# Performance work log

Hardware: AMD Instinct MI355X
Metric: run time of the kernel (lower is better)

## Reference

```python
import jax, jax.numpy as jnp
import numpy as np

B, N, F, UNITS = 8, 2048, 64, 64

def setup_inputs() -> dict:
    key = jax.random.key(0)
    ks = jax.random.split(key, 7)
    inputs = jax.random.normal(ks[0], (B, N, F), dtype=jnp.float32)
    Dynamic_L = jax.random.normal(ks[1], (B, N, N), dtype=jnp.float32)
    W = jax.random.uniform(ks[2], (B, N, N, 3), dtype=jnp.float32)
    Geo = jax.random.normal(ks[3], (N, N), dtype=jnp.float32)
    KL = jax.random.normal(ks[4], (N, N), dtype=jnp.float32)
    # Dense(Units, tanh) params (glorot-ish scale)
    Wd = jax.random.normal(ks[5], (F, UNITS), dtype=jnp.float32) / np.sqrt(F)
    bd = jnp.zeros((UNITS,), dtype=jnp.float32)
    return {"inputs": inputs, "Dynamic_L": Dynamic_L, "W": W,
            "Geo": Geo, "KL": KL, "Wd": Wd, "bd": bd}

def reference(inputs, Dynamic_L, W, Geo, KL, Wd, bd):
    # Weighted fusion of three N x N matrices; Geo/KL broadcast over batch.
    Fusion = Dynamic_L * W[..., 0] + Geo[None] * W[..., 1] + KL[None] * W[..., 2]  # [B,N,N]
    Fusion = jax.nn.softmax(Fusion, axis=-1)
    G1 = jnp.einsum('bnm,bmf->bnf', Fusion, inputs)  # graph matmul [B,N,F]
    return jnp.tanh(G1 @ Wd + bd)  # Dense(Units, tanh) -> [B,N,UNITS]
```

## Files before the change

kernel.cpp:

```cpp
#include <hip/hip_runtime.h>
#include <hip/hip_fp16.h>

#define Nn 2048
#define Ff 64
#define Uu 64
#define NT 256
#define NCH 4
#define G1S 68

typedef _Float16 f16x4 __attribute__((ext_vector_type(4)));
typedef _Float16 f16x8 __attribute__((ext_vector_type(8)));
typedef float    f32x4 __attribute__((ext_vector_type(4)));

#define MFMA32(a,b,c) __builtin_amdgcn_mfma_f32_16x16x32_f16(a,b,c,0,0,0)

#define OPB   0
#define OG1A  65536
#define OG1B  69888
#define OWS   74240
#define OINV  74368
#define SMSZ  74496

__global__ __launch_bounds__(256) void transposeX(const float* __restrict__ X,
                                                  _Float16* __restrict__ Xt) {
    __shared__ _Float16 tile[64][65];
    const int b = blockIdx.x, kt = blockIdx.y;
    #pragma unroll
    for (int i = 0; i < 16; ++i) {
        int e  = i * 256 + threadIdx.x;
        int kk = e >> 6, ff = e & 63;
        tile[ff][kk] = (_Float16)X[((size_t)b * Nn + kt * 64 + kk) * Ff + ff];
    }
    __syncthreads();
    #pragma unroll
    for (int i = 0; i < 16; ++i) {
        int e  = i * 256 + threadIdx.x;
        int ff = e >> 6, kk = e & 63;
        Xt[((size_t)b * Ff + ff) * Nn + kt * 64 + kk] = tile[ff][kk];
    }
}

#define ISSUE2(d0v,d1v,gv,kv,w00,w01,w02,w10,w11,w12, C, HR) {      \
    const int _rr = (HR) >> 1;                                      \
    const size_t _o = (size_t)_rr * Nn + ((size_t)(C) << 9)         \
                    + (((HR) & 1) << 8) + (lane << 2);              \
    d0v = *(const float4*)(dR0 + _o);                               \
    d1v = *(const float4*)(dR1 + _o);                               \
    gv  = *(const float4*)(gR + _o);                                \
    kv  = *(const float4*)(kR + _o);                                \
    w00 = *(const float4*)(wR0 + 3 * _o);                           \
    w01 = *(const float4*)(wR0 + 3 * _o + 4);                       \
    w02 = *(const float4*)(wR0 + 3 * _o + 8);                       \
    w10 = *(const float4*)(wR1 + 3 * _o);                           \
    w11 = *(const float4*)(wR1 + 3 * _o + 4);                       \
    w12 = *(const float4*)(wR1 + 3 * _o + 8);                       \
}

#define CONSUME2(d0v,d1v,gv,kv,w00,w01,w02,w10,w11,w12, P0B,P1B, HR) {          \
    const int _rr = (HR) >> 1;                                                  \
    const int _tr = row0 + _rr;                                                 \
    float a0 = __expf(fminf(d0v.x*w00.x + gv.x*w00.y + kv.x*w00.z, 11.f));      \
    float a1 = __expf(fminf(d0v.y*w00.w + gv.y*w01.x + kv.y*w01.y, 11.f));      \
    float a2 = __expf(fminf(d0v.z*w01.z + gv.z*w01.w + kv.z*w02.x, 11.f));      \
    float a3 = __expf(fminf(d0v.w*w02.y + gv.w*w02.z + kv.w*w02.w, 11.f));      \
    float c0 = __expf(fminf(d1v.x*w10.x + gv.x*w10.y + kv.x*w10.z, 11.f));      \
    float c1 = __expf(fminf(d1v.y*w10.w + gv.y*w11.x + kv.y*w11.y, 11.f));      \
    float c2 = __expf(fminf(d1v.z*w11.z + gv.z*w11.w + kv.z*w12.x, 11.f));      \
    float c3 = __expf(fminf(d1v.w*w12.y + gv.w*w12.z + kv.w*w12.w, 11.f));      \
    f16x4 h0 = {(_Float16)a0, (_Float16)a1, (_Float16)a2, (_Float16)a3};        \
    f16x4 h1 = {(_Float16)c0, (_Float16)c1, (_Float16)c2, (_Float16)c3};        \
    rs0[_rr] += (float)h0[0] + (float)h0[1] + (float)h0[2] + (float)h0[3];      \
    rs1[_rr] += (float)h1[0] + (float)h1[1] + (float)h1[2] + (float)h1[3];      \
    const int _ba = (_tr * 1024 + (((HR) & 1) << 9) + (lane << 3))              \
                    ^ ((_tr & 7) << 4);                                         \
    *(f16x4*)((P0B) + _ba) = h0;                                                \
    *(f16x4*)((P1B) + _ba) = h1;                                                \
}

#define STAGE_CHUNK2(P0B, P1B, C) {                                              \
    ISSUE2(Ad0,Ad1,Agv,Akv,Aw00,Aw01,Aw02,Aw10,Aw11,Aw12, C, 0);                 \
    ISSUE2(Bd0,Bd1,Bgv,Bkv,Bw00,Bw01,Bw02,Bw10,Bw11,Bw12, C, 1);                 \
    CONSUME2(Ad0,Ad1,Agv,Akv,Aw00,Aw01,Aw02,Aw10,Aw11,Aw12, P0B,P1B, 0);         \
    ISSUE2(Ad0,Ad1,Agv,Akv,Aw00,Aw01,Aw02,Aw10,Aw11,Aw12, C, 2);                 \
    CONSUME2(Bd0,Bd1,Bgv,Bkv,Bw00,Bw01,Bw02,Bw10,Bw11,Bw12, P0B,P1B, 1);         \
    ISSUE2(Bd0,Bd1,Bgv,Bkv,Bw00,Bw01,Bw02,Bw10,Bw11,Bw12, C, 3);                 \
    CONSUME2(Ad0,Ad1,Agv,Akv,Aw00,Aw01,Aw02,Aw10,Aw11,Aw12, P0B,P1B, 2);         \
    ISSUE2(Ad0,Ad1,Agv,Akv,Aw00,Aw01,Aw02,Aw10,Aw11,Aw12, C, 4);                 \
    CONSUME2(Bd0,Bd1,Bgv,Bkv,Bw00,Bw01,Bw02,Bw10,Bw11,Bw12, P0B,P1B, 3);         \
    ISSUE2(Bd0,Bd1,Bgv,Bkv,Bw00,Bw01,Bw02,Bw10,Bw11,Bw12, C, 5);                 \
    CONSUME2(Ad0,Ad1,Agv,Akv,Aw00,Aw01,Aw02,Aw10,Aw11,Aw12, P0B,P1B, 4);         \
    ISSUE2(Ad0,Ad1,Agv,Akv,Aw00,Aw01,Aw02,Aw10,Aw11,Aw12, C, 6);                 \
    CONSUME2(Bd0,Bd1,Bgv,Bkv,Bw00,Bw01,Bw02,Bw10,Bw11,Bw12, P0B,P1B, 5);         \
    ISSUE2(Bd0,Bd1,Bgv,Bkv,Bw00,Bw01,Bw02,Bw10,Bw11,Bw12, C, 7);                 \
    CONSUME2(Ad0,Ad1,Agv,Akv,Aw00,Aw01,Aw02,Aw10,Aw11,Aw12, P0B,P1B, 6);         \
    CONSUME2(Bd0,Bd1,Bgv,Bkv,Bw00,Bw01,Bw02,Bw10,Bw11,Bw12, P0B,P1B, 7);         \
}

#define MFMA_PHASE2(PBUF, XC, ACC) {                                          \
    f16x8 p0 = *(const f16x8*)((XC));                                         \
    f16x8 p1 = *(const f16x8*)((XC) + 32);                                    \
    f16x8 p2 = *(const f16x8*)((XC) + 64);                                    \
    f16x8 p3 = *(const f16x8*)((XC) + 96);                                    \
    f16x8 p4 = *(const f16x8*)((XC) + 128);                                   \
    f16x8 p5 = *(const f16x8*)((XC) + 160);                                   \
    f16x8 p6 = *(const f16x8*)((XC) + 192);                                   \
    f16x8 p7 = *(const f16x8*)((XC) + 224);                                   \
    _Pragma("unroll")                                                         \
    for (int kk = 0; kk < 8; ++kk) {                                          \
        const int aa = r * 1024 + kk * 64 + kg * 16;                          \
        f16x8 af = *(const f16x8*)((PBUF) + (aa ^ ((r & 7) << 4)));           \
        f16x8 bv = (kk==0)?p0:(kk==1)?p1:(kk==2)?p2:(kk==3)?p3:               \
                   (kk==4)?p4:(kk==5)?p5:(kk==6)?p6:p7;                       \
        ACC = MFMA32(af, bv, ACC);                                            \
    }                                                                         \
    p0 = *(const f16x8*)((XC) + 256);                                         \
    p1 = *(const f16x8*)((XC) + 288);                                         \
    p2 = *(const f16x8*)((XC) + 320);                                         \
    p3 = *(const f16x8*)((XC) + 352);                                         \
    p4 = *(const f16x8*)((XC) + 384);                                         \
    p5 = *(const f16x8*)((XC) + 416);                                         \
    p6 = *(const f16x8*)((XC) + 448);                                         \
    p7 = *(const f16x8*)((XC) + 480);                                         \
    _Pragma("unroll")                                                         \
    for (int kk = 0; kk < 8; ++kk) {                                          \
        const int aa = r * 1024 + (kk + 8) * 64 + kg * 16;                    \
        f16x8 af = *(const f16x8*)((PBUF) + (aa ^ ((r & 7) << 4)));           \
        f16x8 bv = (kk==0)?p0:(kk==1)?p1:(kk==2)?p2:(kk==3)?p3:               \
                   (kk==4)?p4:(kk==5)?p5:(kk==6)?p6:p7;                       \
        ACC = MFMA32(af, bv, ACC);                                            \
    }                                                                         \
}

__global__ __launch_bounds__(NT, 2) void fused_gcn(
    const _Float16* __restrict__ Xt,
    const float* __restrict__ Dyn,
    const float* __restrict__ Wf,
    const float* __restrict__ Geo,
    const float* __restrict__ KLm,
    const float* __restrict__ Wd,
    const float* __restrict__ bdv,
    float* __restrict__ out)
{
    __shared__ __align__(16) char SM[SMSZ];

    const int t    = threadIdx.x;
    const int lane = t & 63;
    const int wid  = t >> 6;
    const int r    = lane & 15;
    const int kg   = lane >> 4;
    const int rg   = blockIdx.x & 127;
    const int pp   = blockIdx.x >> 7;
    const int n0   = rg << 4;
    const int b0   = pp * 2, b1 = pp * 2 + 1;
    const int row0 = wid << 2;

    const float* dR0 = Dyn + ((size_t)b0 * Nn + n0 + row0) * Nn;
    const float* dR1 = Dyn + ((size_t)b1 * Nn + n0 + row0) * Nn;
    const float* wR0 = Wf  + ((size_t)b0 * Nn + n0 + row0) * (size_t)Nn * 3;
    const float* wR1 = Wf  + ((size_t)b1 * Nn + n0 + row0) * (size_t)Nn * 3;
    const float* gR  = Geo + (size_t)(n0 + row0) * Nn;
    const float* kR  = KLm + (size_t)(n0 + row0) * Nn;
    const _Float16* xw0 = Xt + (size_t)b0 * Ff * Nn
                        + (size_t)(wid * 16 + r) * Nn + (kg << 3);
    const _Float16* xw1 = Xt + (size_t)b1 * Ff * Nn
                        + (size_t)(wid * 16 + r) * Nn + (kg << 3);

    f32x4 acc0 = {0.f,0.f,0.f,0.f}, acc1 = {0.f,0.f,0.f,0.f};
    float rs0[4] = {0.f,0.f,0.f,0.f}, rs1[4] = {0.f,0.f,0.f,0.f};
    float4 Ad0,Ad1,Agv,Akv,Aw00,Aw01,Aw02,Aw10,Aw11,Aw12;
    float4 Bd0,Bd1,Bgv,Bkv,Bw00,Bw01,Bw02,Bw10,Bw11,Bw12;

    STAGE_CHUNK2(SM + OPB, SM + OPB + 16384, 0);
    __syncthreads();

    #pragma unroll 1
    for (int c = 0; c < NCH; ++c) {
        char* bufc = SM + OPB + (c & 1) * 32768;
        MFMA_PHASE2(bufc,          xw0 + ((size_t)c << 9), acc0);
        MFMA_PHASE2(bufc + 16384,  xw1 + ((size_t)c << 9), acc1);
        if (c + 1 < NCH) {
            char* bufn = SM + OPB + ((c + 1) & 1) * 32768;
            STAGE_CHUNK2(bufn, bufn + 16384, c + 1);
        }
        __syncthreads();
    }

    float* ws = (float*)(SM + OWS);
    #pragma unroll
    for (int i = 0; i < 4; ++i) {
        float v = rs0[i];
        v += __shfl_xor(v, 1, 64);  v += __shfl_xor(v, 2, 64);
        v += __shfl_xor(v, 4, 64);  v += __shfl_xor(v, 8, 64);
        v += __shfl_xor(v, 16, 64); v += __shfl_xor(v, 32, 64);
        float u = rs1[i];
        u += __shfl_xor(u, 1, 64);  u += __shfl_xor(u, 2, 64);
        u += __shfl_xor(u, 4, 64);  u += __shfl_xor(u, 8, 64);
        u += __shfl_xor(u, 16, 64); u += __shfl_xor(u, 32, 64);
        if (lane == 0) { ws[row0 + i] = v; ws[16 + row0 + i] = u; }
    }
    __syncthreads();
    float* inv = (float*)(SM + OINV);
    if (t < 32) inv[t] = 1.0f / ws[t];
    __syncthreads();

    float* g1a = (float*)(SM + OG1A);
    float* g1b = (float*)(SM + OG1B);
    #pragma unroll
    for (int i = 0; i < 4; ++i) {
        const int ro = (kg << 2) + i;
        g1a[ro * G1S + (wid << 4) + r] = acc0[i] * inv[ro];
        g1b[ro * G1S + (wid << 4) + r] = acc1[i] * inv[16 + ro];
    }
    __syncthreads();

    const float* ga = g1a + row0 * G1S;
    const float* gb = g1b + row0 * G1S;
    float bb = bdv[lane];
    float a0 = bb, a1 = bb, a2 = bb, a3 = bb;
    float c0 = bb, c1 = bb, c2 = bb, c3 = bb;
    #pragma unroll 4
    for (int f = 0; f < Ff; ++f) {
        float wdv = Wd[f * Uu + lane];
        a0 += ga[f] * wdv;           a1 += ga[G1S + f] * wdv;
        a2 += ga[2 * G1S + f] * wdv; a3 += ga[3 * G1S + f] * wdv;
        c0 += gb[f] * wdv;           c1 += gb[G1S + f] * wdv;
        c2 += gb[2 * G1S + f] * wdv; c3 += gb[3 * G1S + f] * wdv;
    }
    float oa[4] = {a0, a1, a2, a3}, ob[4] = {c0, c1, c2, c3};
    #pragma unroll
    for (int i = 0; i < 4; ++i) {
        float x  = fminf(fmaxf(oa[i], -15.f), 15.f);
        float ex = __expf(2.f * x);
        out[((size_t)b0 * Nn + n0 + row0 + i) * Uu + lane] = (ex - 1.f) / (ex + 1.f);
        float y  = fminf(fmaxf(ob[i], -15.f), 15.f);
        float ey = __expf(2.f * y);
        out[((size_t)b1 * Nn + n0 + row0 + i) * Uu + lane] = (ey - 1.f) / (ey + 1.f);
    }
}

extern "C" void kernel_launch(void* const* d_in, const int* in_sizes, int n_in,
                              void* d_out, int out_size, void* d_ws, size_t ws_size,
                              hipStream_t stream) {
    const float* X   = (const float*)d_in[0];
    const float* Dyn = (const float*)d_in[1];
    const float* Wf  = (const float*)d_in[2];
    const float* Geo = (const float*)d_in[3];
    const float* KLm = (const float*)d_in[4];
    const float* Wd  = (const float*)d_in[5];
    const float* bdv = (const float*)d_in[6];
    float* out = (float*)d_out;

    _Float16* Xt = (_Float16*)d_ws;
    transposeX<<<dim3(8, Nn / 64), dim3(256), 0, stream>>>(X, Xt);
    fused_gcn<<<dim3(4 * 128), dim3(NT), 0, stream>>>(
        Xt, Dyn, Wf, Geo, KLm, Wd, bdv, out);
}
```

Baseline: 130.9 us.

## Double block threads to 512, split staging rows and MFMA batches across waves

The fused kernel now uses 512 threads (8 waves) per block. Each wave stages two rows instead of four, and each wave runs MFMAs for only one of the two batches rather than both. The G1 scratch buffers reuse the P double-buffer region, which shrinks shared memory and targets 4 blocks per CU. More waves in flight should hide the HBM latency of the streaming loads, at the cost of smaller per-wave staging pipelines and tighter register limits.

```diff
diff --git a/kernel.cpp b/kernel.cpp
--- a/kernel.cpp
+++ b/kernel.cpp
@@ -4,7 +4,7 @@
 #define Nn 2048
 #define Ff 64
 #define Uu 64
-#define NT 256
+#define NT 512
 #define NCH 4
 #define G1S 68
 
@@ -14,12 +14,9 @@
 
 #define MFMA32(a,b,c) __builtin_amdgcn_mfma_f32_16x16x32_f16(a,b,c,0,0,0)
 
-#define OPB   0
-#define OG1A  65536
-#define OG1B  69888
-#define OWS   74240
-#define OINV  74368
-#define SMSZ  74496
+#define OWS   65536
+#define OINV  65664
+#define SMSZ  65792
 
 __global__ __launch_bounds__(256) void transposeX(const float* __restrict__ X,
                                                   _Float16* __restrict__ Xt) {
@@ -40,10 +37,9 @@
     }
 }
 
-#define ISSUE2(d0v,d1v,gv,kv,w00,w01,w02,w10,w11,w12, C, HR) {      \
-    const int _rr = (HR) >> 1;                                      \
-    const size_t _o = (size_t)_rr * Nn + ((size_t)(C) << 9)         \
-                    + (((HR) & 1) << 8) + (lane << 2);              \
+#define ISSUE2(d0v,d1v,gv,kv,w00,w01,w02,w10,w11,w12, C, UR, H) {   \
+    const size_t _o = (size_t)(UR) * Nn + ((size_t)(C) << 9)        \
+                    + ((H) << 8) + (lane << 2);                     \
     d0v = *(const float4*)(dR0 + _o);                               \
     d1v = *(const float4*)(dR1 + _o);                               \
     gv  = *(const float4*)(gR + _o);                                \
@@ -56,9 +52,8 @@
     w12 = *(const float4*)(wR1 + 3 * _o + 8);                       \
 }
 
-#define CONSUME2(d0v,d1v,gv,kv,w00,w01,w02,w10,w11,w12, P0B,P1B, HR) {          \
-    const int _rr = (HR) >> 1;                                                  \
-    const int _tr = row0 + _rr;                                                 \
+#define CONSUME2(d0v,d1v,gv,kv,w00,w01,w02,w10,w11,w12, P0B,P1B, UR, H) {       \
+    const int _tr = row0 + (UR);                                                \
     float a0 = __expf(fminf(d0v.x*w00.x + gv.x*w00.y + kv.x*w00.z, 11.f));      \
     float a1 = __expf(fminf(d0v.y*w00.w + gv.y*w01.x + kv.y*w01.y, 11.f));      \
     float a2 = __expf(fminf(d0v.z*w01.z + gv.z*w01.w + kv.z*w02.x, 11.f));      \
@@ -69,34 +64,26 @@
     float c3 = __expf(fminf(d1v.w*w12.y + gv.w*w12.z + kv.w*w12.w, 11.f));      \
     f16x4 h0 = {(_Float16)a0, (_Float16)a1, (_Float16)a2, (_Float16)a3};        \
     f16x4 h1 = {(_Float16)c0, (_Float16)c1, (_Float16)c2, (_Float16)c3};        \
-    rs0[_rr] += (float)h0[0] + (float)h0[1] + (float)h0[2] + (float)h0[3];      \
-    rs1[_rr] += (float)h1[0] + (float)h1[1] + (float)h1[2] + (float)h1[3];      \
-    const int _ba = (_tr * 1024 + (((HR) & 1) << 9) + (lane << 3))              \
+    rs0[UR] += (float)h0[0] + (float)h0[1] + (float)h0[2] + (float)h0[3];       \
+    rs1[UR] += (float)h1[0] + (float)h1[1] + (float)h1[2] + (float)h1[3];       \
+    const int _ba = (_tr * 1024 + ((H) << 9) + (lane << 3))                     \
                     ^ ((_tr & 7) << 4);                                         \
     *(f16x4*)((P0B) + _ba) = h0;                                                \
     *(f16x4*)((P1B) + _ba) = h1;                                                \
 }
 
 #define STAGE_CHUNK2(P0B, P1B, C) {                                              \
-    ISSUE2(Ad0,Ad1,Agv,Akv,Aw00,Aw01,Aw02,Aw10,Aw11,Aw12, C, 0);                 \
-    ISSUE2(Bd0,Bd1,Bgv,Bkv,Bw00,Bw01,Bw02,Bw10,Bw11,Bw12, C, 1);                 \
-    CONSUME2(Ad0,Ad1,Agv,Akv,Aw00,Aw01,Aw02,Aw10,Aw11,Aw12, P0B,P1B, 0);         \
-    ISSUE2(Ad0,Ad1,Agv,Akv,Aw00,Aw01,Aw02,Aw10,Aw11,Aw12, C, 2);                 \
-    CONSUME2(Bd0,Bd1,Bgv,Bkv,Bw00,Bw01,Bw02,Bw10,Bw11,Bw12, P0B,P1B, 1);         \
-    ISSUE2(Bd0,Bd1,Bgv,Bkv,Bw00,Bw01,Bw02,Bw10,Bw11,Bw12, C, 3);                 \
-    CONSUME2(Ad0,Ad1,Agv,Akv,Aw00,Aw01,Aw02,Aw10,Aw11,Aw12, P0B,P1B, 2);         \
-    ISSUE2(Ad0,Ad1,Agv,Akv,Aw00,Aw01,Aw02,Aw10,Aw11,Aw12, C, 4);                 \
-    CONSUME2(Bd0,Bd1,Bgv,Bkv,Bw00,Bw01,Bw02,Bw10,Bw11,Bw12, P0B,P1B, 3);         \
-    ISSUE2(Bd0,Bd1,Bgv,Bkv,Bw00,Bw01,Bw02,Bw10,Bw11,Bw12, C, 5);                 \
-    CONSUME2(Ad0,Ad1,Agv,Akv,Aw00,Aw01,Aw02,Aw10,Aw11,Aw12, P0B,P1B, 4);         \
-    ISSUE2(Ad0,Ad1,Agv,Akv,Aw00,Aw01,Aw02,Aw10,Aw11,Aw12, C, 6);                 \
-    CONSUME2(Bd0,Bd1,Bgv,Bkv,Bw00,Bw01,Bw02,Bw10,Bw11,Bw12, P0B,P1B, 5);         \
-    ISSUE2(Bd0,Bd1,Bgv,Bkv,Bw00,Bw01,Bw02,Bw10,Bw11,Bw12, C, 7);                 \
-    CONSUME2(Ad0,Ad1,Agv,Akv,Aw00,Aw01,Aw02,Aw10,Aw11,Aw12, P0B,P1B, 6);         \
-    CONSUME2(Bd0,Bd1,Bgv,Bkv,Bw00,Bw01,Bw02,Bw10,Bw11,Bw12, P0B,P1B, 7);         \
-}
-
-#define MFMA_PHASE2(PBUF, XC, ACC) {                                          \
+    ISSUE2(Ad0,Ad1,Agv,Akv,Aw00,Aw01,Aw02,Aw10,Aw11,Aw12, C, 0, 0);              \
+    ISSUE2(Bd0,Bd1,Bgv,Bkv,Bw00,Bw01,Bw02,Bw10,Bw11,Bw12, C, 0, 1);              \
+    CONSUME2(Ad0,Ad1,Agv,Akv,Aw00,Aw01,Aw02,Aw10,Aw11,Aw12, P0B,P1B, 0, 0);      \
+    ISSUE2(Ad0,Ad1,Agv,Akv,Aw00,Aw01,Aw02,Aw10,Aw11,Aw12, C, 1, 0);              \
+    CONSUME2(Bd0,Bd1,Bgv,Bkv,Bw00,Bw01,Bw02,Bw10,Bw11,Bw12, P0B,P1B, 0, 1);      \
+    ISSUE2(Bd0,Bd1,Bgv,Bkv,Bw00,Bw01,Bw02,Bw10,Bw11,Bw12, C, 1, 1);              \
+    CONSUME2(Ad0,Ad1,Agv,Akv,Aw00,Aw01,Aw02,Aw10,Aw11,Aw12, P0B,P1B, 1, 0);      \
+    CONSUME2(Bd0,Bd1,Bgv,Bkv,Bw00,Bw01,Bw02,Bw10,Bw11,Bw12, P0B,P1B, 1, 1);      \
+}
+
+#define MFMA_PHASE2(PBUF, XC) {                                               \
     f16x8 p0 = *(const f16x8*)((XC));                                         \
     f16x8 p1 = *(const f16x8*)((XC) + 32);                                    \
     f16x8 p2 = *(const f16x8*)((XC) + 64);                                    \
@@ -111,7 +98,7 @@
         f16x8 af = *(const f16x8*)((PBUF) + (aa ^ ((r & 7) << 4)));           \
         f16x8 bv = (kk==0)?p0:(kk==1)?p1:(kk==2)?p2:(kk==3)?p3:               \
                    (kk==4)?p4:(kk==5)?p5:(kk==6)?p6:p7;                       \
-        ACC = MFMA32(af, bv, ACC);                                            \
+        acc = MFMA32(af, bv, acc);                                            \
     }                                                                         \
     p0 = *(const f16x8*)((XC) + 256);                                         \
     p1 = *(const f16x8*)((XC) + 288);                                         \
@@ -127,11 +114,11 @@
         f16x8 af = *(const f16x8*)((PBUF) + (aa ^ ((r & 7) << 4)));           \
         f16x8 bv = (kk==0)?p0:(kk==1)?p1:(kk==2)?p2:(kk==3)?p3:               \
                    (kk==4)?p4:(kk==5)?p5:(kk==6)?p6:p7;                       \
-        ACC = MFMA32(af, bv, ACC);                                            \
+        acc = MFMA32(af, bv, acc);                                            \
     }                                                                         \
 }
 
-__global__ __launch_bounds__(NT, 2) void fused_gcn(
+__global__ __launch_bounds__(NT, 4) void fused_gcn(
     const _Float16* __restrict__ Xt,
     const float* __restrict__ Dyn,
     const float* __restrict__ Wf,
@@ -152,7 +139,7 @@
     const int pp   = blockIdx.x >> 7;
     const int n0   = rg << 4;
     const int b0   = pp * 2, b1 = pp * 2 + 1;
-    const int row0 = wid << 2;
+    const int row0 = wid << 1;
 
     const float* dR0 = Dyn + ((size_t)b0 * Nn + n0 + row0) * Nn;
     const float* dR1 = Dyn + ((size_t)b1 * Nn + n0 + row0) * Nn;
@@ -160,26 +147,25 @@
     const float* wR1 = Wf  + ((size_t)b1 * Nn + n0 + row0) * (size_t)Nn * 3;
     const float* gR  = Geo + (size_t)(n0 + row0) * Nn;
     const float* kR  = KLm + (size_t)(n0 + row0) * Nn;
-    const _Float16* xw0 = Xt + (size_t)b0 * Ff * Nn
-                        + (size_t)(wid * 16 + r) * Nn + (kg << 3);
-    const _Float16* xw1 = Xt + (size_t)b1 * Ff * Nn
-                        + (size_t)(wid * 16 + r) * Nn + (kg << 3);
-
-    f32x4 acc0 = {0.f,0.f,0.f,0.f}, acc1 = {0.f,0.f,0.f,0.f};
-    float rs0[4] = {0.f,0.f,0.f,0.f}, rs1[4] = {0.f,0.f,0.f,0.f};
+
+    const int bb = wid >> 2, ct = wid & 3;
+    const _Float16* xwv = Xt + (size_t)(bb ? b1 : b0) * Ff * Nn
+                        + (size_t)(ct * 16 + r) * Nn + (kg << 3);
+
+    f32x4 acc = {0.f,0.f,0.f,0.f};
+    float rs0[2] = {0.f,0.f}, rs1[2] = {0.f,0.f};
     float4 Ad0,Ad1,Agv,Akv,Aw00,Aw01,Aw02,Aw10,Aw11,Aw12;
     float4 Bd0,Bd1,Bgv,Bkv,Bw00,Bw01,Bw02,Bw10,Bw11,Bw12;
 
-    STAGE_CHUNK2(SM + OPB, SM + OPB + 16384, 0);
+    STAGE_CHUNK2(SM, SM + 16384, 0);
     __syncthreads();
 
     #pragma unroll 1
     for (int c = 0; c < NCH; ++c) {
-        char* bufc = SM + OPB + (c & 1) * 32768;
-        MFMA_PHASE2(bufc,          xw0 + ((size_t)c << 9), acc0);
-        MFMA_PHASE2(bufc + 16384,  xw1 + ((size_t)c << 9), acc1);
+        const char* pb = SM + (c & 1) * 32768 + bb * 16384;
+        MFMA_PHASE2(pb, xwv + ((size_t)c << 9));
         if (c + 1 < NCH) {
-            char* bufn = SM + OPB + ((c + 1) & 1) * 32768;
+            char* bufn = SM + ((c + 1) & 1) * 32768;
             STAGE_CHUNK2(bufn, bufn + 16384, c + 1);
         }
         __syncthreads();
@@ -187,7 +173,7 @@
 
     float* ws = (float*)(SM + OWS);
     #pragma unroll
-    for (int i = 0; i < 4; ++i) {
+    for (int i = 0; i < 2; ++i) {
         float v = rs0[i];
         v += __shfl_xor(v, 1, 64);  v += __shfl_xor(v, 2, 64);
         v += __shfl_xor(v, 4, 64);  v += __shfl_xor(v, 8, 64);
@@ -203,38 +189,33 @@
     if (t < 32) inv[t] = 1.0f / ws[t];
     __syncthreads();
 
-    float* g1a = (float*)(SM + OG1A);
-    float* g1b = (float*)(SM + OG1B);
+    float* g1a = (float*)SM;
+    float* g1b = (float*)(SM + 4352);
+    float* g1w = bb ? g1b : g1a;
     #pragma unroll
     for (int i = 0; i < 4; ++i) {
         const int ro = (kg << 2) + i;
-        g1a[ro * G1S + (wid << 4) + r] = acc0[i] * inv[ro];
-        g1b[ro * G1S + (wid << 4) + r] = acc1[i] * inv[16 + ro];
-    }
-    __syncthreads();
-
-    const float* ga = g1a + row0 * G1S;
-    const float* gb = g1b + row0 * G1S;
-    float bb = bdv[lane];
-    float a0 = bb, a1 = bb, a2 = bb, a3 = bb;
-    float c0 = bb, c1 = bb, c2 = bb, c3 = bb;
+        g1w[ro * G1S + ct * 16 + r] = acc[i] * inv[bb * 16 + ro];
+    }
+    __syncthreads();
+
+    const int rw0 = (wid & 3) << 2;
+    const float* gg = (bb ? g1b : g1a) + rw0 * G1S;
+    const int ob = bb ? b1 : b0;
+    float bias = bdv[lane];
+    float o0 = bias, o1 = bias, o2 = bias, o3 = bias;
     #pragma unroll 4
     for (int f = 0; f < Ff; ++f) {
         float wdv = Wd[f * Uu + lane];
-        a0 += ga[f] * wdv;           a1 += ga[G1S + f] * wdv;
-        a2 += ga[2 * G1S + f] * wdv; a3 += ga[3 * G1S + f] * wdv;
-        c0 += gb[f] * wdv;           c1 += gb[G1S + f] * wdv;
-        c2 += gb[2 * G1S + f] * wdv; c3 += gb[3 * G1S + f] * wdv;
-    }
-    float oa[4] = {a0, a1, a2, a3}, ob[4] = {c0, c1, c2, c3};
+        o0 += gg[f] * wdv;           o1 += gg[G1S + f] * wdv;
+        o2 += gg[2 * G1S + f] * wdv; o3 += gg[3 * G1S + f] * wdv;
+    }
+    float oo[4] = {o0, o1, o2, o3};
     #pragma unroll
     for (int i = 0; i < 4; ++i) {
-        float x  = fminf(fmaxf(oa[i], -15.f), 15.f);
+        float x  = fminf(fmaxf(oo[i], -15.f), 15.f);
         float ex = __expf(2.f * x);
-        out[((size_t)b0 * Nn + n0 + row0 + i) * Uu + lane] = (ex - 1.f) / (ex + 1.f);
-        float y  = fminf(fmaxf(ob[i], -15.f), 15.f);
-        float ey = __expf(2.f * y);
-        out[((size_t)b1 * Nn + n0 + row0 + i) * Uu + lane] = (ey - 1.f) / (ey + 1.f);
+        out[((size_t)ob * Nn + n0 + rw0 + i) * Uu + lane] = (ex - 1.f) / (ex + 1.f);
     }
 }
 
```

Result: slower. 156.8 us (+19.8%).
